# Kernel tuning notes

Hardware: AMD Instinct MI355X
Metric: run time of the kernel (lower is better)

Reference implementation:

```python
import jax, jax.numpy as jnp
import numpy as np

N_NODES = 50000
N_EDGES = 1600000
D_FEAT = 32


def setup_inputs() -> dict:
    key = jax.random.key(0)
    k1, k2, k3, k4 = jax.random.split(key, 4)
    node_feat = jax.random.normal(k1, (N_NODES, D_FEAT), dtype=jnp.float32)
    edge_feat = jax.random.normal(k2, (N_EDGES, D_FEAT), dtype=jnp.float32)
    eps = jnp.zeros((1,), dtype=jnp.float32)  # learnable eps, init 0
    src = jax.random.randint(k3, (N_EDGES,), 0, N_NODES, dtype=jnp.int64)
    dst = jax.random.randint(k4, (N_EDGES,), 0, N_NODES, dtype=jnp.int64)
    return {"node_feat": node_feat, "edge_feat": edge_feat, "eps": eps,
            "src": src, "dst": dst}


def reference(node_feat, edge_feat, eps, src, dst):
    # message: relu(h_src + h_edge) per edge  [E, D]
    m = jax.nn.relu(node_feat[src] + edge_feat)
    # sum-aggregate messages into destination nodes  [N, D]
    neigh = jax.ops.segment_sum(m, dst, num_segments=node_feat.shape[0])
    # eps-scaled residual
    return (1.0 + eps[0]) * node_feat + neigh
```

## Files before the change

### kernel.cpp

```cpp
#include <hip/hip_runtime.h>

#define N_NODES 50000
#define N_EDGES 1600000
#define D_FEAT 32
#define SCAN_BLOCK 1024
#define N_SCAN_BLOCKS ((N_NODES + SCAN_BLOCK - 1) / SCAN_BLOCK)

#define WS_CNT   0
#define WS_EXCL  (N_NODES)
#define WS_BSUM  (2 * N_NODES)
#define WS_BSUMX (2 * N_NODES + 64)
#define WS_RANK  (2 * N_NODES + 128)
#define WS_PAIR  (2 * N_NODES + 128 + N_EDGES)

typedef float f4 __attribute__((ext_vector_type(4)));


__global__ void hist_rank(const int* __restrict__ dst,
                          int* __restrict__ cnt,
                          int* __restrict__ rank) {
    int e = blockIdx.x * blockDim.x + threadIdx.x;
    if (e < N_EDGES) rank[e] = atomicAdd(&cnt[dst[e]], 1);
}

__global__ void scan_blocks(const int* __restrict__ cnt,
                            int* __restrict__ excl,
                            int* __restrict__ bsum) {
    __shared__ int lds[SCAN_BLOCK];
    int tid = threadIdx.x;
    int i = blockIdx.x * SCAN_BLOCK + tid;
    int v = (i < N_NODES) ? cnt[i] : 0;
    int sum = v;
    lds[tid] = v;
    __syncthreads();
    for (int ofs = 1; ofs < SCAN_BLOCK; ofs <<= 1) {
        int t = (tid >= ofs) ? lds[tid - ofs] : 0;
        __syncthreads();
        sum += t;
        lds[tid] = sum;
        __syncthreads();
    }
    if (i < N_NODES) excl[i] = sum - v;
    if (tid == SCAN_BLOCK - 1) bsum[blockIdx.x] = lds[SCAN_BLOCK - 1];
}

__global__ void scan_bsums(const int* __restrict__ bsum, int* __restrict__ bsumx) {
    int lane = threadIdx.x;
    int orig = (lane < N_SCAN_BLOCKS) ? bsum[lane] : 0;
    int v = orig;
    for (int o = 1; o < 64; o <<= 1) {
        int t = __shfl_up(v, o);
        if (lane >= o) v += t;
    }
    if (lane < N_SCAN_BLOCKS) bsumx[lane] = v - orig;
}

__global__ void scatter_pairs(const int* __restrict__ src,
                              const int* __restrict__ dst,
                              const int* __restrict__ excl,
                              const int* __restrict__ bsumx,
                              const int* __restrict__ rank,
                              int2* __restrict__ pair) {
    int e = blockIdx.x * blockDim.x + threadIdx.x;
    if (e >= N_EDGES) return;
    int d = dst[e];
    int pos = excl[d] + bsumx[d >> 10] + rank[e];
    pair[pos] = make_int2(e, src[e]);
}

__global__ void reduce_gather(const float* __restrict__ node_feat,
                              const float* __restrict__ edge_feat,
                              const float* __restrict__ eps,
                              const int* __restrict__ excl,
                              const int* __restrict__ bsumx,
                              const int* __restrict__ cnt,
                              const int2* __restrict__ pair,
                              float* __restrict__ out) {
    int t = blockIdx.x * blockDim.x + threadIdx.x;
    int n = t >> 3;
    int g = t & 7;
    if (n >= N_NODES) return;

    int start = excl[n] + bsumx[n >> 10];
    int c = cnt[n];
    int gbase = (threadIdx.x & 63) & ~7;

    const f4* efp = (const f4*)edge_feat;
    const f4* nfp = (const f4*)node_feat;

    f4 acc = (f4)(0.f);
    int i0 = 0;
    for (; i0 + 8 <= c; i0 += 8) {
        int2 p = pair[start + i0 + g];
#pragma unroll
        for (int j = 0; j < 8; ++j) {
            int e = __shfl(p.x, gbase + j);
            int s = __shfl(p.y, gbase + j);
            f4 ef = __builtin_nontemporal_load(&efp[(size_t)e * 8 + g]);
            f4 nf = nfp[(size_t)s * 8 + g];
            acc.x += fmaxf(nf.x + ef.x, 0.f);
            acc.y += fmaxf(nf.y + ef.y, 0.f);
            acc.z += fmaxf(nf.z + ef.z, 0.f);
            acc.w += fmaxf(nf.w + ef.w, 0.f);
        }
    }
    int rem = c - i0;
    if (rem > 0) {
        int2 p = (g < rem) ? pair[start + i0 + g] : make_int2(0, 0);
        for (int j = 0; j < rem; ++j) {
            int e = __shfl(p.x, gbase + j);
            int s = __shfl(p.y, gbase + j);
            f4 ef = __builtin_nontemporal_load(&efp[(size_t)e * 8 + g]);
            f4 nf = nfp[(size_t)s * 8 + g];
            acc.x += fmaxf(nf.x + ef.x, 0.f);
            acc.y += fmaxf(nf.y + ef.y, 0.f);
            acc.z += fmaxf(nf.z + ef.z, 0.f);
            acc.w += fmaxf(nf.w + ef.w, 0.f);
        }
    }

    float scale = 1.0f + eps[0];
    f4 h = nfp[(size_t)n * 8 + g];
    f4 o;
    o.x = scale * h.x + acc.x;
    o.y = scale * h.y + acc.y;
    o.z = scale * h.z + acc.z;
    o.w = scale * h.w + acc.w;
    ((f4*)out)[(size_t)n * 8 + g] = o;
}


__global__ void fb_init_out(const float* __restrict__ node_feat,
                            const float* __restrict__ eps,
                            float* __restrict__ out) {
    int i = blockIdx.x * blockDim.x + threadIdx.x;
    const int n4 = N_NODES * D_FEAT / 4;
    float scale = 1.0f + eps[0];
    if (i < n4) {
        float4 v = ((const float4*)node_feat)[i];
        v.x *= scale; v.y *= scale; v.z *= scale; v.w *= scale;
        ((float4*)out)[i] = v;
    }
}

__global__ void fb_scatter(const float* __restrict__ node_feat,
                           const float* __restrict__ edge_feat,
                           const int* __restrict__ src,
                           const int* __restrict__ dst,
                           float* __restrict__ out) {
    int t = blockIdx.x * blockDim.x + threadIdx.x;
    int e = t >> 3;
    int g = t & 7;
    if (e >= N_EDGES) return;
    int s = src[e];
    int d = dst[e];
    float4 nf = ((const float4*)node_feat)[s * 8 + g];
    float4 ef = ((const float4*)edge_feat)[(size_t)e * 8 + g];
    float* op = out + (size_t)d * D_FEAT + g * 4;
    unsafeAtomicAdd(op + 0, fmaxf(nf.x + ef.x, 0.f));
    unsafeAtomicAdd(op + 1, fmaxf(nf.y + ef.y, 0.f));
    unsafeAtomicAdd(op + 2, fmaxf(nf.z + ef.z, 0.f));
    unsafeAtomicAdd(op + 3, fmaxf(nf.w + ef.w, 0.f));
}

extern "C" void kernel_launch(void* const* d_in, const int* in_sizes, int n_in,
                              void* d_out, int out_size, void* d_ws, size_t ws_size,
                              hipStream_t stream) {
    const float* node_feat = (const float*)d_in[0];
    const float* edge_feat = (const float*)d_in[1];
    const float* eps       = (const float*)d_in[2];
    const int*   src       = (const int*)d_in[3];
    const int*   dst       = (const int*)d_in[4];
    float* out = (float*)d_out;

    const int B = 256;
    const size_t need = ((size_t)WS_PAIR + 2ull * N_EDGES) * sizeof(int);

    if (ws_size < need) {
        int n4 = N_NODES * D_FEAT / 4;
        fb_init_out<<<(n4 + B - 1) / B, B, 0, stream>>>(node_feat, eps, out);
        long long total = (long long)N_EDGES * 8;
        fb_scatter<<<(int)((total + B - 1) / B), B, 0, stream>>>(
            node_feat, edge_feat, src, dst, out);
        return;
    }

    int* ws = (int*)d_ws;
    int*  cnt   = ws + WS_CNT;
    int*  excl  = ws + WS_EXCL;
    int*  bsum  = ws + WS_BSUM;
    int*  bsumx = ws + WS_BSUMX;
    int*  rank  = ws + WS_RANK;
    int2* pair  = (int2*)(ws + WS_PAIR);

    hipMemsetAsync(cnt, 0, N_NODES * sizeof(int), stream);

    hist_rank<<<(N_EDGES + B - 1) / B, B, 0, stream>>>(dst, cnt, rank);
    scan_blocks<<<N_SCAN_BLOCKS, SCAN_BLOCK, 0, stream>>>(cnt, excl, bsum);
    scan_bsums<<<1, 64, 0, stream>>>(bsum, bsumx);

    scatter_pairs<<<(N_EDGES + B - 1) / B, B, 0, stream>>>(
        src, dst, excl, bsumx, rank, pair);

    long long ntotal = (long long)N_NODES * 8;
    reduce_gather<<<(int)((ntotal + B - 1) / B), B, 0, stream>>>(
        node_feat, edge_feat, eps, excl, bsumx, cnt, pair, out);
}
```

Baseline: 434.7 us.

## Replace rank array with partitioned atomic-cursor scatter and prefetch pairs in gather

Drops the per-edge rank array. The histogram reads dst four at a time, and a new finalize pass writes absolute offsets. The scatter instead partitions destination nodes into eight ranges, and each block group claims slots via atomic cursors, which is meant to localize pair writes and atomics. The gather loop is merged into one masked loop that prefetches the next pair chunk. In exchange, edge order per node becomes nondeterministic, and every block reads src/dst once per partition.

```diff
diff --git a/kernel.cpp b/kernel.cpp
--- a/kernel.cpp
+++ b/kernel.cpp
@@ -5,22 +5,29 @@
 #define D_FEAT 32
 #define SCAN_BLOCK 1024
 #define N_SCAN_BLOCKS ((N_NODES + SCAN_BLOCK - 1) / SCAN_BLOCK)
+#define NPART 8
+#define PART_SIZE ((N_NODES + NPART - 1) / NPART)
+#define SCATTER_BLOCKS 2048
 
 #define WS_CNT   0
 #define WS_EXCL  (N_NODES)
-#define WS_BSUM  (2 * N_NODES)
-#define WS_BSUMX (2 * N_NODES + 64)
-#define WS_RANK  (2 * N_NODES + 128)
-#define WS_PAIR  (2 * N_NODES + 128 + N_EDGES)
+#define WS_OM    (2 * N_NODES)
+#define WS_BSUM  (3 * N_NODES)
+#define WS_BSUMX (3 * N_NODES + 64)
+#define WS_PAIR  (3 * N_NODES + 128)
 
 typedef float f4 __attribute__((ext_vector_type(4)));
 
 
-__global__ void hist_rank(const int* __restrict__ dst,
-                          int* __restrict__ cnt,
-                          int* __restrict__ rank) {
-    int e = blockIdx.x * blockDim.x + threadIdx.x;
-    if (e < N_EDGES) rank[e] = atomicAdd(&cnt[dst[e]], 1);
+__global__ void hist(const int* __restrict__ dst, int* __restrict__ cnt) {
+    int q = blockIdx.x * blockDim.x + threadIdx.x;
+    const int NQ = N_EDGES / 4;
+    if (q >= NQ) return;
+    int4 d4 = ((const int4*)dst)[q];
+    atomicAdd(&cnt[d4.x], 1);
+    atomicAdd(&cnt[d4.y], 1);
+    atomicAdd(&cnt[d4.z], 1);
+    atomicAdd(&cnt[d4.w], 1);
 }
 
 __global__ void scan_blocks(const int* __restrict__ cnt,
@@ -55,17 +62,32 @@
     if (lane < N_SCAN_BLOCKS) bsumx[lane] = v - orig;
 }
 
+__global__ void finalize_off(const int* __restrict__ excl,
+                             const int* __restrict__ bsumx,
+                             int* __restrict__ om) {
+    int i = blockIdx.x * SCAN_BLOCK + threadIdx.x;
+    if (i < N_NODES) om[i] = excl[i] + bsumx[blockIdx.x];
+}
+
 __global__ void scatter_pairs(const int* __restrict__ src,
                               const int* __restrict__ dst,
-                              const int* __restrict__ excl,
-                              const int* __restrict__ bsumx,
-                              const int* __restrict__ rank,
+                              int* __restrict__ om,
                               int2* __restrict__ pair) {
-    int e = blockIdx.x * blockDim.x + threadIdx.x;
-    if (e >= N_EDGES) return;
-    int d = dst[e];
-    int pos = excl[d] + bsumx[d >> 10] + rank[e];
-    pair[pos] = make_int2(e, src[e]);
+    int part = blockIdx.x & (NPART - 1);
+    int lo = part * PART_SIZE;
+    int hi = lo + PART_SIZE;
+    int bi = blockIdx.x >> 3;
+    const int nb = SCATTER_BLOCKS / NPART;
+    const int NQ = N_EDGES / 4;
+    for (int q = bi * blockDim.x + threadIdx.x; q < NQ; q += nb * blockDim.x) {
+        int4 d4 = ((const int4*)dst)[q];
+        int4 s4 = ((const int4*)src)[q];
+        int e0 = q * 4;
+        if (d4.x >= lo && d4.x < hi) pair[atomicAdd(&om[d4.x], 1)] = make_int2(e0,     s4.x);
+        if (d4.y >= lo && d4.y < hi) pair[atomicAdd(&om[d4.y], 1)] = make_int2(e0 + 1, s4.y);
+        if (d4.z >= lo && d4.z < hi) pair[atomicAdd(&om[d4.z], 1)] = make_int2(e0 + 2, s4.z);
+        if (d4.w >= lo && d4.w < hi) pair[atomicAdd(&om[d4.w], 1)] = make_int2(e0 + 3, s4.w);
+    }
 }
 
 __global__ void reduce_gather(const float* __restrict__ node_feat,
@@ -89,34 +111,32 @@
     const f4* nfp = (const f4*)node_feat;
 
     f4 acc = (f4)(0.f);
-    int i0 = 0;
-    for (; i0 + 8 <= c; i0 += 8) {
-        int2 p = pair[start + i0 + g];
+
+    int idx0 = start + g;
+    if (idx0 > N_EDGES - 1) idx0 = N_EDGES - 1;
+    int2 p = pair[idx0];
+
+    for (int i0 = 0; i0 < c; i0 += 8) {
+        int idxn = start + i0 + 8 + g;
+        if (idxn > N_EDGES - 1) idxn = N_EDGES - 1;
+        int2 pn = pair[idxn];
+
+        int lim = c - i0;
+        if (lim > 8) lim = 8;
 #pragma unroll
         for (int j = 0; j < 8; ++j) {
-            int e = __shfl(p.x, gbase + j);
-            int s = __shfl(p.y, gbase + j);
-            f4 ef = __builtin_nontemporal_load(&efp[(size_t)e * 8 + g]);
-            f4 nf = nfp[(size_t)s * 8 + g];
-            acc.x += fmaxf(nf.x + ef.x, 0.f);
-            acc.y += fmaxf(nf.y + ef.y, 0.f);
-            acc.z += fmaxf(nf.z + ef.z, 0.f);
-            acc.w += fmaxf(nf.w + ef.w, 0.f);
+            if (j < lim) {
+                int e = __shfl(p.x, gbase + j);
+                int s = __shfl(p.y, gbase + j);
+                f4 ef = __builtin_nontemporal_load(&efp[(size_t)e * 8 + g]);
+                f4 nf = nfp[(size_t)s * 8 + g];
+                acc.x += fmaxf(nf.x + ef.x, 0.f);
+                acc.y += fmaxf(nf.y + ef.y, 0.f);
+                acc.z += fmaxf(nf.z + ef.z, 0.f);
+                acc.w += fmaxf(nf.w + ef.w, 0.f);
+            }
         }
-    }
-    int rem = c - i0;
-    if (rem > 0) {
-        int2 p = (g < rem) ? pair[start + i0 + g] : make_int2(0, 0);
-        for (int j = 0; j < rem; ++j) {
-            int e = __shfl(p.x, gbase + j);
-            int s = __shfl(p.y, gbase + j);
-            f4 ef = __builtin_nontemporal_load(&efp[(size_t)e * 8 + g]);
-            f4 nf = nfp[(size_t)s * 8 + g];
-            acc.x += fmaxf(nf.x + ef.x, 0.f);
-            acc.y += fmaxf(nf.y + ef.y, 0.f);
-            acc.z += fmaxf(nf.z + ef.z, 0.f);
-            acc.w += fmaxf(nf.w + ef.w, 0.f);
-        }
+        p = pn;
     }
 
     float scale = 1.0f + eps[0];
@@ -188,19 +208,20 @@
     int* ws = (int*)d_ws;
     int*  cnt   = ws + WS_CNT;
     int*  excl  = ws + WS_EXCL;
+    int*  om    = ws + WS_OM;
     int*  bsum  = ws + WS_BSUM;
     int*  bsumx = ws + WS_BSUMX;
-    int*  rank  = ws + WS_RANK;
     int2* pair  = (int2*)(ws + WS_PAIR);
 
     hipMemsetAsync(cnt, 0, N_NODES * sizeof(int), stream);
 
-    hist_rank<<<(N_EDGES + B - 1) / B, B, 0, stream>>>(dst, cnt, rank);
+    int nq = N_EDGES / 4;
+    hist<<<(nq + B - 1) / B, B, 0, stream>>>(dst, cnt);
     scan_blocks<<<N_SCAN_BLOCKS, SCAN_BLOCK, 0, stream>>>(cnt, excl, bsum);
     scan_bsums<<<1, 64, 0, stream>>>(bsum, bsumx);
-
-    scatter_pairs<<<(N_EDGES + B - 1) / B, B, 0, stream>>>(
-        src, dst, excl, bsumx, rank, pair);
+    finalize_off<<<N_SCAN_BLOCKS, SCAN_BLOCK, 0, stream>>>(excl, bsumx, om);
+
+    scatter_pairs<<<SCATTER_BLOCKS, B, 0, stream>>>(src, dst, om, pair);
 
     long long ntotal = (long long)N_NODES * 8;
     reduce_gather<<<(int)((ntotal + B - 1) / B), B, 0, stream>>>(
```

After: 465.7 us. 7.1% more time.

## Replace global-atomic counting sort with LDS-partitioned histogram and scatter

Applied to the files above, without the earlier changes.

The global-atomic histogram/rank pass and the rank-based scatter are replaced by a two-level counting sort. Node ids are split into 8 partitions of 6250 and edges into 32 stripes. Each block builds a per-stripe histogram in LDS for its partition, then scatters (edge, src) pairs using LDS atomic cursors seeded from per-stripe prefix bases. This removes 1.6M global atomics and the rank array. In exchange each block rereads its whole stripe of dst once per partition, several small kernels are added, and the grid is only 256 blocks, which may leave much of the GPU idle.

```diff
diff --git a/kernel.cpp b/kernel.cpp
--- a/kernel.cpp
+++ b/kernel.cpp
@@ -5,22 +5,52 @@
 #define D_FEAT 32
 #define SCAN_BLOCK 1024
 #define N_SCAN_BLOCKS ((N_NODES + SCAN_BLOCK - 1) / SCAN_BLOCK)
-
-#define WS_CNT   0
-#define WS_EXCL  (N_NODES)
-#define WS_BSUM  (2 * N_NODES)
-#define WS_BSUMX (2 * N_NODES + 64)
-#define WS_RANK  (2 * N_NODES + 128)
-#define WS_PAIR  (2 * N_NODES + 128 + N_EDGES)
+#define NPART 8
+#define PART_SIZE (N_NODES / NPART)
+#define NSTRIPE 32
+#define NQ (N_EDGES / 4)
+#define NQB (NQ / NSTRIPE)
+
+#define WS_BCNT  0
+#define WS_OFFB  (32 * N_NODES)
+#define WS_CNT   (64 * N_NODES)
+#define WS_EXCL  (65 * N_NODES)
+#define WS_OFF   (66 * N_NODES)
+#define WS_BSUM  (67 * N_NODES + 64)
+#define WS_BSUMX (67 * N_NODES + 128)
+#define WS_PAIR  (67 * N_NODES + 192)
 
 typedef float f4 __attribute__((ext_vector_type(4)));
 
 
-__global__ void hist_rank(const int* __restrict__ dst,
-                          int* __restrict__ cnt,
-                          int* __restrict__ rank) {
-    int e = blockIdx.x * blockDim.x + threadIdx.x;
-    if (e < N_EDGES) rank[e] = atomicAdd(&cnt[dst[e]], 1);
+__global__ void hist_part(const int* __restrict__ dst, int* __restrict__ bcnt) {
+    __shared__ int lh[PART_SIZE];
+    int p = blockIdx.x & (NPART - 1);
+    int ib = blockIdx.x >> 3;
+    int lo = p * PART_SIZE;
+    for (int k = threadIdx.x; k < PART_SIZE; k += blockDim.x) lh[k] = 0;
+    __syncthreads();
+    const int4* dq = (const int4*)dst;
+    int q0 = ib * NQB;
+    for (int q = q0 + threadIdx.x; q < q0 + NQB; q += blockDim.x) {
+        int4 d4 = dq[q];
+        if ((unsigned)(d4.x - lo) < (unsigned)PART_SIZE) atomicAdd(&lh[d4.x - lo], 1);
+        if ((unsigned)(d4.y - lo) < (unsigned)PART_SIZE) atomicAdd(&lh[d4.y - lo], 1);
+        if ((unsigned)(d4.z - lo) < (unsigned)PART_SIZE) atomicAdd(&lh[d4.z - lo], 1);
+        if ((unsigned)(d4.w - lo) < (unsigned)PART_SIZE) atomicAdd(&lh[d4.w - lo], 1);
+    }
+    __syncthreads();
+    for (int k = threadIdx.x; k < PART_SIZE; k += blockDim.x)
+        bcnt[ib * N_NODES + lo + k] = lh[k];
+}
+
+__global__ void sum_bcnt(const int* __restrict__ bcnt, int* __restrict__ cnt) {
+    int n = blockIdx.x * blockDim.x + threadIdx.x;
+    if (n >= N_NODES) return;
+    int s = 0;
+#pragma unroll
+    for (int i = 0; i < NSTRIPE; ++i) s += bcnt[i * N_NODES + n];
+    cnt[n] = s;
 }
 
 __global__ void scan_blocks(const int* __restrict__ cnt,
@@ -55,24 +85,61 @@
     if (lane < N_SCAN_BLOCKS) bsumx[lane] = v - orig;
 }
 
-__global__ void scatter_pairs(const int* __restrict__ src,
-                              const int* __restrict__ dst,
-                              const int* __restrict__ excl,
-                              const int* __restrict__ bsumx,
-                              const int* __restrict__ rank,
-                              int2* __restrict__ pair) {
-    int e = blockIdx.x * blockDim.x + threadIdx.x;
-    if (e >= N_EDGES) return;
-    int d = dst[e];
-    int pos = excl[d] + bsumx[d >> 10] + rank[e];
-    pair[pos] = make_int2(e, src[e]);
+__global__ void finalize_off(const int* __restrict__ excl,
+                             const int* __restrict__ bsumx,
+                             int* __restrict__ off) {
+    int i = blockIdx.x * SCAN_BLOCK + threadIdx.x;
+    if (i < N_NODES) off[i] = excl[i] + bsumx[blockIdx.x];
+    else if (i == N_NODES) off[i] = N_EDGES;
+}
+
+__global__ void block_bases(const int* __restrict__ off,
+                            const int* __restrict__ bcnt,
+                            int* __restrict__ offb) {
+    int n = blockIdx.x * blockDim.x + threadIdx.x;
+    if (n >= N_NODES) return;
+    int run = off[n];
+#pragma unroll
+    for (int i = 0; i < NSTRIPE; ++i) {
+        offb[i * N_NODES + n] = run;
+        run += bcnt[i * N_NODES + n];
+    }
+}
+
+__global__ void scatter_part(const int* __restrict__ src,
+                             const int* __restrict__ dst,
+                             const int* __restrict__ offb,
+                             int2* __restrict__ pair) {
+    __shared__ int cur[PART_SIZE];
+    int p = blockIdx.x & (NPART - 1);
+    int ib = blockIdx.x >> 3;
+    int lo = p * PART_SIZE;
+    for (int k = threadIdx.x; k < PART_SIZE; k += blockDim.x)
+        cur[k] = offb[ib * N_NODES + lo + k];
+    __syncthreads();
+    const int4* dq = (const int4*)dst;
+    const int4* sq = (const int4*)src;
+    int q0 = ib * NQB;
+    for (int q = q0 + threadIdx.x; q < q0 + NQB; q += blockDim.x) {
+        int4 d4 = dq[q];
+        bool ax = (unsigned)(d4.x - lo) < (unsigned)PART_SIZE;
+        bool ay = (unsigned)(d4.y - lo) < (unsigned)PART_SIZE;
+        bool az = (unsigned)(d4.z - lo) < (unsigned)PART_SIZE;
+        bool aw = (unsigned)(d4.w - lo) < (unsigned)PART_SIZE;
+        if (!(ax | ay | az | aw)) continue;
+        int4 s4 = sq[q];
+        int e0 = q * 4;
+        if (ax) { int pos = atomicAdd(&cur[d4.x - lo], 1); pair[pos] = make_int2(e0,     s4.x); }
+        if (ay) { int pos = atomicAdd(&cur[d4.y - lo], 1); pair[pos] = make_int2(e0 + 1, s4.y); }
+        if (az) { int pos = atomicAdd(&cur[d4.z - lo], 1); pair[pos] = make_int2(e0 + 2, s4.z); }
+        if (aw) { int pos = atomicAdd(&cur[d4.w - lo], 1); pair[pos] = make_int2(e0 + 3, s4.w); }
+    }
 }
 
 __global__ void reduce_gather(const float* __restrict__ node_feat,
                               const float* __restrict__ edge_feat,
                               const float* __restrict__ eps,
-                              const int* __restrict__ excl,
-                              const int* __restrict__ bsumx,
+                              const int* __restrict__ off,
                               const int* __restrict__ cnt,
                               const int2* __restrict__ pair,
                               float* __restrict__ out) {
@@ -81,7 +148,7 @@
     int g = t & 7;
     if (n >= N_NODES) return;
 
-    int start = excl[n] + bsumx[n >> 10];
+    int start = off[n];
     int c = cnt[n];
     int gbase = (threadIdx.x & 63) & ~7;
 
@@ -186,23 +253,25 @@
     }
 
     int* ws = (int*)d_ws;
+    int*  bcnt  = ws + WS_BCNT;
+    int*  offb  = ws + WS_OFFB;
     int*  cnt   = ws + WS_CNT;
     int*  excl  = ws + WS_EXCL;
+    int*  off   = ws + WS_OFF;
     int*  bsum  = ws + WS_BSUM;
     int*  bsumx = ws + WS_BSUMX;
-    int*  rank  = ws + WS_RANK;
     int2* pair  = (int2*)(ws + WS_PAIR);
 
-    hipMemsetAsync(cnt, 0, N_NODES * sizeof(int), stream);
-
-    hist_rank<<<(N_EDGES + B - 1) / B, B, 0, stream>>>(dst, cnt, rank);
+    hist_part<<<NPART * NSTRIPE, B, 0, stream>>>(dst, bcnt);
+    sum_bcnt<<<(N_NODES + B - 1) / B, B, 0, stream>>>(bcnt, cnt);
     scan_blocks<<<N_SCAN_BLOCKS, SCAN_BLOCK, 0, stream>>>(cnt, excl, bsum);
     scan_bsums<<<1, 64, 0, stream>>>(bsum, bsumx);
-
-    scatter_pairs<<<(N_EDGES + B - 1) / B, B, 0, stream>>>(
-        src, dst, excl, bsumx, rank, pair);
+    finalize_off<<<N_SCAN_BLOCKS, SCAN_BLOCK, 0, stream>>>(excl, bsumx, off);
+    block_bases<<<(N_NODES + B - 1) / B, B, 0, stream>>>(off, bcnt, offb);
+
+    scatter_part<<<NPART * NSTRIPE, B, 0, stream>>>(src, dst, offb, pair);
 
     long long ntotal = (long long)N_NODES * 8;
     reduce_gather<<<(int)((ntotal + B - 1) / B), B, 0, stream>>>(
-        node_feat, edge_feat, eps, excl, bsumx, cnt, pair, out);
-}
+        node_feat, edge_feat, eps, off, cnt, pair, out);
+}
```

Result: slower. 444.3 us (+2.2%).
